# Kernel tuning notes

Hardware: AMD Instinct MI355X
Metric: run time of the kernel (lower is better)

Reference implementation:

```python
import jax, jax.numpy as jnp
import numpy as np

B, C, H, W = 512, 3, 64, 32
K = 2                      # fractional pool kernel size
HOUT, WOUT = 38, 16        # floor(64*0.6), floor(32*0.5)
HID = 128                  # RNN hidden size
D = C * HOUT               # RNN input size = 114


def _frac_starts(in_size, out_size, k, u=0.5):
    # PyTorch fractional-max-pool interval formula with deterministic sample u
    alpha = (in_size - k) / (out_size - 1)
    i = np.arange(out_size - 1)
    starts = np.floor((i + u) * alpha) - np.floor(u * alpha)
    return np.concatenate([starts, [in_size - k]]).astype(np.int32)

ROW = _frac_starts(H, HOUT, K)   # (HOUT,) window start rows
COL = _frac_starts(W, WOUT, K)   # (WOUT,) window start cols


def setup_inputs() -> dict:
    key = jax.random.key(0)
    ks = jax.random.split(key, 5)
    s = 1.0 / np.sqrt(HID)  # torch RNNCell init scale
    return {
        "x": jax.random.normal(ks[0], (B, C, H, W), jnp.float32),
        "W_ih": jax.random.uniform(ks[1], (HID, D), jnp.float32, -s, s),
        "W_hh": jax.random.uniform(ks[2], (HID, HID), jnp.float32, -s, s),
        "b_ih": jax.random.uniform(ks[3], (HID,), jnp.float32, -s, s),
        "b_hh": jax.random.uniform(ks[4], (HID,), jnp.float32, -s, s),
    }


def reference(x, W_ih, W_hh, b_ih, b_hh):
    # 1) fractional max pool, kernel 2: pairwise max over gathered window starts
    xr = jnp.maximum(x[:, :, ROW, :], x[:, :, ROW + 1, :])          # (B,C,HOUT,W)
    pooled = jnp.maximum(xr[:, :, :, COL], xr[:, :, :, COL + 1])    # (B,C,HOUT,WOUT)
    # 2) exact (erf-based) GELU, matching torch nn.GELU default
    act = jax.nn.gelu(pooled, approximate=False)
    # 3) sequence over width: (WOUT, B, C*HOUT), C-major flatten matches torch view
    seq = act.transpose(3, 0, 1, 2).reshape(WOUT, B, D)
    # 4) vanilla RNNCell across time via scan
    def step(h, xt):
        h = jnp.tanh(xt @ W_ih.T + b_ih + h @ W_hh.T + b_hh)
        return h, h
    _, outs = jax.lax.scan(step, jnp.zeros((B, HID), x.dtype), seq)  # (WOUT,B,HID)
    # 5) temporal mean + tanh
    t_mean = jnp.tanh(outs.mean(axis=0))                             # (B,HID)
    # 6) modulate by global spatial mean of pooled; torch broadcasting of
    #    (B,HID) * (B,1,1,1) yields (B,1,B,HID) — replicated faithfully
    s_mean = pooled.mean(axis=(1, 2, 3), keepdims=True)              # (B,1,1,1)
    return t_mean * s_mean                                           # (B,1,B,HID)
```

## Files before the change

kernel.cpp:

```cpp
#include <hip/hip_runtime.h>
#include <math.h>

#define BB   512
#define CC   3
#define HH   64
#define WW   32
#define HOUT 38
#define WOUT 16
#define HID  128
#define DD   114
#define SEQP 120
#define WIHP 120
#define WHHP 132
#define NPOOL (CC*HOUT*WOUT)

typedef float f32x4 __attribute__((ext_vector_type(4)));

__device__ __forceinline__ float fast_tanh(float u) {
    return 1.f - 2.f / (__expf(2.f * u) + 1.f);
}

#define WS_SMEAN 0
#define WS_TMEAN 512

__global__ __launch_bounds__(256, 2)
void k1_fused(const float* __restrict__ x,
              const float* __restrict__ Wih,
              const float* __restrict__ Whh,
              const float* __restrict__ bih,
              const float* __restrict__ bhh,
              float* __restrict__ s_mean,
              float* __restrict__ t_mean)
{
    __shared__ __align__(16) float wst[HID * WIHP];
    __shared__ __align__(16) float seq[WOUT][SEQP];
    __shared__ __align__(16) float Zl[WOUT][HID];
    __shared__ __align__(16) float hbuf[2][HID];
    __shared__ float psum[HID];
    __shared__ float red[4];
    __shared__ int   rowl[HOUT];

    const int tid  = threadIdx.x;
    const int half = tid >> 7;
    const int k    = tid & 127;
    const int wid  = tid >> 6;
    const int lane = tid & 63;
    const int b    = blockIdx.x;

    if (tid < HOUT) {
        double alpha = (double)(HH - 2) / (double)(HOUT - 1);
        rowl[tid] = (tid < HOUT - 1)
            ? (int)(floor((tid + 0.5) * alpha) - floor(0.5 * alpha))
            : (HH - 2);
    }
    if (tid < HID) hbuf[0][tid] = 0.f;
    if (tid < 96)  seq[tid / 6][DD + tid % 6] = 0.f;

    {
        const f32x4* xg = (const f32x4*)(x + (size_t)b * (CC*HH*WW));
        f32x4*       xd = (f32x4*)wst;
        #pragma unroll
        for (int i = 0; i < (CC*HH*WW/4)/256; ++i)
            xd[tid + 256*i] = xg[tid + 256*i];
    }
    __syncthreads();

    float ps = 0.f;
    #pragma unroll
    for (int it = 0; it < 8; ++it) {
        int idx = tid + it*256;
        if (idx < NPOOL) {
            int c  = idx / (HOUT*WOUT);
            int r  = idx % (HOUT*WOUT);
            int ho = r / WOUT;
            int wo = r % WOUT;
            const float* p0 = &wst[c*(HH*WW) + rowl[ho]*WW + 2*wo];
            float m = fmaxf(fmaxf(p0[0], p0[1]), fmaxf(p0[WW], p0[WW+1]));
            ps += m;
            seq[wo][c*HOUT + ho] =
                0.5f * m * (1.f + erff(m * 0.70710678118654752440f));
        }
    }
    #pragma unroll
    for (int off = 32; off > 0; off >>= 1) ps += __shfl_down(ps, off);
    if (lane == 0) red[wid] = ps;
    __syncthreads();
    if (tid == 0)
        s_mean[b] = (red[0] + red[1] + red[2] + red[3]) * (1.f / (float)NPOOL);

    {
        const f32x4* g4 = (const f32x4*)Wih;
        for (int j4 = tid; j4 < (HID*DD)/4; j4 += 256) {
            f32x4 v = g4[j4];
            int j = 4*j4;
            #pragma unroll
            for (int e = 0; e < 4; ++e) {
                int r  = (j + e) / DD;
                int cc = (j + e) - r*DD;
                wst[r*WIHP + cc] = v[e];
            }
        }
        for (int j = tid; j < HID*6; j += 256)
            wst[(j/6)*WIHP + DD + (j % 6)] = 0.f;
    }
    __syncthreads();
    f32x4 wih[15];
    {
        const f32x4* wr = (const f32x4*)&wst[k*WIHP + half*60];
        #pragma unroll
        for (int dd = 0; dd < 15; ++dd) wih[dd] = wr[dd];
    }

    float zreg[WOUT];
    #pragma unroll
    for (int t = 0; t < WOUT; ++t) {
        const f32x4* a4 = (const f32x4*)&seq[t][half*60];
        float s0 = 0.f, s1 = 0.f, s2 = 0.f, s3 = 0.f;
        #pragma unroll
        for (int dd = 0; dd < 15; ++dd) {
            f32x4 a = a4[dd];
            s0 = fmaf(wih[dd].x, a.x, s0);
            s1 = fmaf(wih[dd].y, a.y, s1);
            s2 = fmaf(wih[dd].z, a.z, s2);
            s3 = fmaf(wih[dd].w, a.w, s3);
        }
        float zp = (s0 + s1) + (s2 + s3);
        if (half) Zl[t][k] = zp; else zreg[t] = zp;
    }
    __syncthreads();
    {
        const float bias = bih[k] + bhh[k];
        if (!half) {
            #pragma unroll
            for (int t = 0; t < WOUT; ++t) zreg[t] += bias + Zl[t][k];
        }
    }

    f32x4 whh[16];
    #pragma unroll
    for (int c = 0; c < 2; ++c) {
        const f32x4* g4 = (const f32x4*)(Whh + c*64*HID);
        for (int j4 = tid; j4 < (64*HID)/4; j4 += 256) {
            int r  = j4 >> 5;
            int c4 = j4 & 31;
            *(f32x4*)&wst[r*WHHP + (c4 << 2)] = g4[j4];
        }
        __syncthreads();
        if ((k >> 6) == c) {
            const f32x4* wr = (const f32x4*)&wst[(k & 63)*WHHP + (half << 6)];
            #pragma unroll
            for (int dd = 0; dd < 16; ++dd) whh[dd] = wr[dd];
        }
        __syncthreads();
    }

    float hsum = 0.f;
    #pragma unroll
    for (int t = 0; t < WOUT; ++t) {
        const int cur = t & 1, nxt = cur ^ 1;
        const f32x4* h4 = (const f32x4*)&hbuf[cur][half << 6];
        float s0 = 0.f, s1 = 0.f, s2 = 0.f, s3 = 0.f;
        #pragma unroll
        for (int dd = 0; dd < 16; ++dd) {
            f32x4 hv = h4[dd];
            s0 = fmaf(whh[dd].x, hv.x, s0);
            s1 = fmaf(whh[dd].y, hv.y, s1);
            s2 = fmaf(whh[dd].z, hv.z, s2);
            s3 = fmaf(whh[dd].w, hv.w, s3);
        }
        float up = (s0 + s1) + (s2 + s3);
        if (half) psum[k] = up;
        __syncthreads();
        if (!half) {
            float hn = fast_tanh(zreg[t] + up + psum[k]);
            hsum += hn;
            hbuf[nxt][k] = hn;
        }
        __syncthreads();
    }
    if (!half) t_mean[b*HID + k] = fast_tanh(hsum * (1.f / 16.f));
}

__global__ __launch_bounds__(256)
void k2_out(const float* __restrict__ s_mean,
            const float* __restrict__ t_mean,
            f32x4* __restrict__ out)
{
    const int i   = blockIdx.x >> 3;
    const int sub = blockIdx.x & 7;
    const float s = s_mean[i];
    const f32x4* t4 = (const f32x4*)t_mean + sub*2048;
    f32x4*       o  = out + (size_t)i*16384 + sub*2048;
    const int tid = threadIdx.x;
    #pragma unroll
    for (int j = 0; j < 8; ++j) {
        int idx = tid + j*256;
        o[idx] = s * t4[idx];
    }
}

extern "C" void kernel_launch(void* const* d_in, const int* in_sizes, int n_in,
                              void* d_out, int out_size, void* d_ws, size_t ws_size,
                              hipStream_t stream)
{
    const float* x   = (const float*)d_in[0];
    const float* Wih = (const float*)d_in[1];
    const float* Whh = (const float*)d_in[2];
    const float* bih = (const float*)d_in[3];
    const float* bhh = (const float*)d_in[4];

    float* ws     = (float*)d_ws;
    float* s_mean = ws + WS_SMEAN;
    float* t_mean = ws + WS_TMEAN;

    k1_fused<<<dim3(BB), dim3(256), 0, stream>>>(x, Wih, Whh, bih, bhh, s_mean, t_mean);
    k2_out  <<<dim3(4096), dim3(256), 0, stream>>>(s_mean, t_mean, (f32x4*)d_out);
}
```

Baseline: 52.25 us.

## Run each batch RNN on a single wavefront with direct global-to-LDS weight loads

Rewrites the fused pooling+RNN kernel so each batch item is handled by one 64-lane wavefront instead of 256 threads. Each lane owns two hidden units and holds both W_hh rows in registers, which removes the split-K partial-sum exchange and most block-wide barriers in the recurrence. W_ih is copied to LDS with global_load_lds, and x is read straight from global memory instead of being staged. In exchange, each wave does four times more serial work, register pressure is very high (64 float4 for W_hh plus accumulators), and occupancy depends on 57KB of LDS per 64-thread block.

```diff
diff --git a/kernel.cpp b/kernel.cpp
--- a/kernel.cpp
+++ b/kernel.cpp
@@ -10,72 +10,63 @@
 #define HID  128
 #define DD   114
 #define SEQP 120
-#define WIHP 120
-#define WHHP 132
 #define NPOOL (CC*HOUT*WOUT)
 
 typedef float f32x4 __attribute__((ext_vector_type(4)));
+typedef float f32x2 __attribute__((ext_vector_type(2)));
 
 __device__ __forceinline__ float fast_tanh(float u) {
     return 1.f - 2.f / (__expf(2.f * u) + 1.f);
 }
 
+__device__ __forceinline__ void gl_lds16(const void* g, void* l) {
+    __builtin_amdgcn_global_load_lds(
+        (const __attribute__((address_space(1))) unsigned int*)g,
+        (__attribute__((address_space(3))) unsigned int*)l, 16, 0, 0);
+}
+
 #define WS_SMEAN 0
 #define WS_TMEAN 512
 
-__global__ __launch_bounds__(256, 2)
-void k1_fused(const float* __restrict__ x,
-              const float* __restrict__ Wih,
-              const float* __restrict__ Whh,
-              const float* __restrict__ bih,
-              const float* __restrict__ bhh,
-              float* __restrict__ s_mean,
-              float* __restrict__ t_mean)
+__global__ __launch_bounds__(64, 1)
+void k1_wave(const float* __restrict__ x,
+             const float* __restrict__ Wih,
+             const float* __restrict__ Whh,
+             const float* __restrict__ bih,
+             const float* __restrict__ bhh,
+             float* __restrict__ s_mean,
+             float* __restrict__ t_mean)
 {
-    __shared__ __align__(16) float wst[HID * WIHP];
+    __shared__ __align__(16) float wihl[HID * DD];
     __shared__ __align__(16) float seq[WOUT][SEQP];
-    __shared__ __align__(16) float Zl[WOUT][HID];
     __shared__ __align__(16) float hbuf[2][HID];
-    __shared__ float psum[HID];
-    __shared__ float red[4];
-    __shared__ int   rowl[HOUT];
 
-    const int tid  = threadIdx.x;
-    const int half = tid >> 7;
-    const int k    = tid & 127;
-    const int wid  = tid >> 6;
-    const int lane = tid & 63;
-    const int b    = blockIdx.x;
+    const int l = threadIdx.x;
+    const int b = blockIdx.x;
 
-    if (tid < HOUT) {
-        double alpha = (double)(HH - 2) / (double)(HOUT - 1);
-        rowl[tid] = (tid < HOUT - 1)
-            ? (int)(floor((tid + 0.5) * alpha) - floor(0.5 * alpha))
-            : (HH - 2);
-    }
-    if (tid < HID) hbuf[0][tid] = 0.f;
-    if (tid < 96)  seq[tid / 6][DD + tid % 6] = 0.f;
+    #pragma unroll
+    for (int i = 0; i < 57; ++i)
+        gl_lds16((const char*)Wih + (size_t)(i*64 + l)*16,
+                 (char*)wihl + i*1024);
 
-    {
-        const f32x4* xg = (const f32x4*)(x + (size_t)b * (CC*HH*WW));
-        f32x4*       xd = (f32x4*)wst;
-        #pragma unroll
-        for (int i = 0; i < (CC*HH*WW/4)/256; ++i)
-            xd[tid + 256*i] = xg[tid + 256*i];
-    }
-    __syncthreads();
-
+    const float* xb = x + (size_t)b * (CC*HH*WW);
+    const double alpha = (double)(HH - 2) / (double)(HOUT - 1);
+    const double f05   = floor(0.5 * alpha);
     float ps = 0.f;
     #pragma unroll
-    for (int it = 0; it < 8; ++it) {
-        int idx = tid + it*256;
+    for (int it = 0; it < 29; ++it) {
+        int idx = l + 64*it;
         if (idx < NPOOL) {
             int c  = idx / (HOUT*WOUT);
             int r  = idx % (HOUT*WOUT);
             int ho = r / WOUT;
             int wo = r % WOUT;
-            const float* p0 = &wst[c*(HH*WW) + rowl[ho]*WW + 2*wo];
-            float m = fmaxf(fmaxf(p0[0], p0[1]), fmaxf(p0[WW], p0[WW+1]));
+            int r0 = (ho < HOUT-1) ? (int)(floor((ho + 0.5)*alpha) - f05)
+                                   : (HH - 2);
+            const float* p = xb + c*(HH*WW) + r0*WW + 2*wo;
+            f32x2 u0 = *(const f32x2*)p;
+            f32x2 u1 = *(const f32x2*)(p + WW);
+            float m = fmaxf(fmaxf(u0.x, u0.y), fmaxf(u1.x, u1.y));
             ps += m;
             seq[wo][c*HOUT + ho] =
                 0.5f * m * (1.f + erff(m * 0.70710678118654752440f));
@@ -83,102 +74,90 @@
     }
     #pragma unroll
     for (int off = 32; off > 0; off >>= 1) ps += __shfl_down(ps, off);
-    if (lane == 0) red[wid] = ps;
+    if (l == 0) s_mean[b] = ps * (1.f / (float)NPOOL);
+
+    hbuf[0][l] = 0.f;  hbuf[0][64 + l] = 0.f;
+
     __syncthreads();
-    if (tid == 0)
-        s_mean[b] = (red[0] + red[1] + red[2] + red[3]) * (1.f / (float)NPOOL);
 
+    f32x4 whA[32], whB[32];
     {
-        const f32x4* g4 = (const f32x4*)Wih;
-        for (int j4 = tid; j4 < (HID*DD)/4; j4 += 256) {
-            f32x4 v = g4[j4];
-            int j = 4*j4;
-            #pragma unroll
-            for (int e = 0; e < 4; ++e) {
-                int r  = (j + e) / DD;
-                int cc = (j + e) - r*DD;
-                wst[r*WIHP + cc] = v[e];
-            }
-        }
-        for (int j = tid; j < HID*6; j += 256)
-            wst[(j/6)*WIHP + DD + (j % 6)] = 0.f;
-    }
-    __syncthreads();
-    f32x4 wih[15];
-    {
-        const f32x4* wr = (const f32x4*)&wst[k*WIHP + half*60];
+        const f32x4* ra = (const f32x4*)(Whh + (size_t)l * HID);
+        const f32x4* rb = (const f32x4*)(Whh + (size_t)(l + 64) * HID);
         #pragma unroll
-        for (int dd = 0; dd < 15; ++dd) wih[dd] = wr[dd];
+        for (int j = 0; j < 32; ++j) { whA[j] = ra[j]; whB[j] = rb[j]; }
     }
 
-    float zreg[WOUT];
+    float zA[16], zB[16];
     #pragma unroll
-    for (int t = 0; t < WOUT; ++t) {
-        const f32x4* a4 = (const f32x4*)&seq[t][half*60];
-        float s0 = 0.f, s1 = 0.f, s2 = 0.f, s3 = 0.f;
+    for (int t = 0; t < 16; ++t) { zA[t] = 0.f; zB[t] = 0.f; }
+    #pragma unroll
+    for (int cc = 0; cc < 4; ++cc) {
+        const int d0 = cc * 28;
+        f32x2 wa[14], wb[14];
+        {
+            const f32x2* pa = (const f32x2*)&wihl[l*DD + d0];
+            const f32x2* pb = (const f32x2*)&wihl[(l + 64)*DD + d0];
+            #pragma unroll
+            for (int j = 0; j < 14; ++j) { wa[j] = pa[j]; wb[j] = pb[j]; }
+        }
         #pragma unroll
-        for (int dd = 0; dd < 15; ++dd) {
-            f32x4 a = a4[dd];
-            s0 = fmaf(wih[dd].x, a.x, s0);
-            s1 = fmaf(wih[dd].y, a.y, s1);
-            s2 = fmaf(wih[dd].z, a.z, s2);
-            s3 = fmaf(wih[dd].w, a.w, s3);
-        }
-        float zp = (s0 + s1) + (s2 + s3);
-        if (half) Zl[t][k] = zp; else zreg[t] = zp;
-    }
-    __syncthreads();
-    {
-        const float bias = bih[k] + bhh[k];
-        if (!half) {
+        for (int t = 0; t < 16; ++t) {
+            const f32x4* sv = (const f32x4*)&seq[t][d0];
+            float a0=0.f, a1=0.f, b0=0.f, b1=0.f;
             #pragma unroll
-            for (int t = 0; t < WOUT; ++t) zreg[t] += bias + Zl[t][k];
+            for (int j2 = 0; j2 < 7; ++j2) {
+                f32x4 s = sv[j2];
+                f32x2 wa0 = wa[2*j2], wa1 = wa[2*j2+1];
+                f32x2 wb0 = wb[2*j2], wb1 = wb[2*j2+1];
+                a0 = fmaf(wa0.x, s.x, a0); a1 = fmaf(wa0.y, s.y, a1);
+                a0 = fmaf(wa1.x, s.z, a0); a1 = fmaf(wa1.y, s.w, a1);
+                b0 = fmaf(wb0.x, s.x, b0); b1 = fmaf(wb0.y, s.y, b1);
+                b0 = fmaf(wb1.x, s.z, b0); b1 = fmaf(wb1.y, s.w, b1);
+            }
+            zA[t] += a0 + a1;  zB[t] += b0 + b1;
         }
     }
+    {
+        f32x2 wa = *(const f32x2*)&wihl[l*DD + 112];
+        f32x2 wb = *(const f32x2*)&wihl[(l + 64)*DD + 112];
+        #pragma unroll
+        for (int t = 0; t < 16; ++t) {
+            f32x2 s = *(const f32x2*)&seq[t][112];
+            zA[t] += wa.x*s.x + wa.y*s.y;
+            zB[t] += wb.x*s.x + wb.y*s.y;
+        }
+    }
+    {
+        const float biasA = bih[l]      + bhh[l];
+        const float biasB = bih[l + 64] + bhh[l + 64];
+        #pragma unroll
+        for (int t = 0; t < 16; ++t) { zA[t] += biasA; zB[t] += biasB; }
+    }
 
-    f32x4 whh[16];
+    float hsA = 0.f, hsB = 0.f;
     #pragma unroll
-    for (int c = 0; c < 2; ++c) {
-        const f32x4* g4 = (const f32x4*)(Whh + c*64*HID);
-        for (int j4 = tid; j4 < (64*HID)/4; j4 += 256) {
-            int r  = j4 >> 5;
-            int c4 = j4 & 31;
-            *(f32x4*)&wst[r*WHHP + (c4 << 2)] = g4[j4];
+    for (int t = 0; t < 16; ++t) {
+        const int cur = t & 1, nxt = cur ^ 1;
+        const f32x4* h4 = (const f32x4*)hbuf[cur];
+        float a0=0.f, a1=0.f, a2=0.f, a3=0.f;
+        float b0=0.f, b1=0.f, b2=0.f, b3=0.f;
+        #pragma unroll
+        for (int j = 0; j < 32; ++j) {
+            f32x4 h = h4[j];
+            a0 = fmaf(whA[j].x, h.x, a0); a1 = fmaf(whA[j].y, h.y, a1);
+            a2 = fmaf(whA[j].z, h.z, a2); a3 = fmaf(whA[j].w, h.w, a3);
+            b0 = fmaf(whB[j].x, h.x, b0); b1 = fmaf(whB[j].y, h.y, b1);
+            b2 = fmaf(whB[j].z, h.z, b2); b3 = fmaf(whB[j].w, h.w, b3);
         }
-        __syncthreads();
-        if ((k >> 6) == c) {
-            const f32x4* wr = (const f32x4*)&wst[(k & 63)*WHHP + (half << 6)];
-            #pragma unroll
-            for (int dd = 0; dd < 16; ++dd) whh[dd] = wr[dd];
-        }
+        float hA = fast_tanh(zA[t] + ((a0 + a1) + (a2 + a3)));
+        float hB = fast_tanh(zB[t] + ((b0 + b1) + (b2 + b3)));
+        hsA += hA; hsB += hB;
+        hbuf[nxt][l] = hA;  hbuf[nxt][64 + l] = hB;
         __syncthreads();
     }
-
-    float hsum = 0.f;
-    #pragma unroll
-    for (int t = 0; t < WOUT; ++t) {
-        const int cur = t & 1, nxt = cur ^ 1;
-        const f32x4* h4 = (const f32x4*)&hbuf[cur][half << 6];
-        float s0 = 0.f, s1 = 0.f, s2 = 0.f, s3 = 0.f;
-        #pragma unroll
-        for (int dd = 0; dd < 16; ++dd) {
-            f32x4 hv = h4[dd];
-            s0 = fmaf(whh[dd].x, hv.x, s0);
-            s1 = fmaf(whh[dd].y, hv.y, s1);
-            s2 = fmaf(whh[dd].z, hv.z, s2);
-            s3 = fmaf(whh[dd].w, hv.w, s3);
-        }
-        float up = (s0 + s1) + (s2 + s3);
-        if (half) psum[k] = up;
-        __syncthreads();
-        if (!half) {
-            float hn = fast_tanh(zreg[t] + up + psum[k]);
-            hsum += hn;
-            hbuf[nxt][k] = hn;
-        }
-        __syncthreads();
-    }
-    if (!half) t_mean[b*HID + k] = fast_tanh(hsum * (1.f / 16.f));
+    t_mean[b*HID + l]      = fast_tanh(hsA * (1.f / 16.f));
+    t_mean[b*HID + 64 + l] = fast_tanh(hsB * (1.f / 16.f));
 }
 
 __global__ __launch_bounds__(256)
@@ -213,6 +192,6 @@
     float* s_mean = ws + WS_SMEAN;
     float* t_mean = ws + WS_TMEAN;
 
-    k1_fused<<<dim3(BB), dim3(256), 0, stream>>>(x, Wih, Whh, bih, bhh, s_mean, t_mean);
-    k2_out  <<<dim3(4096), dim3(256), 0, stream>>>(s_mean, t_mean, (f32x4*)d_out);
+    k1_wave<<<dim3(BB), dim3(64), 0, stream>>>(x, Wih, Whh, bih, bhh, s_mean, t_mean);
+    k2_out <<<dim3(4096), dim3(256), 0, stream>>>(s_mean, t_mean, (f32x4*)d_out);
 }
```

Result: slower. 173.6 us (+232.3%).
